# Optimization experiments

Measured on AMD Instinct MI355X. Metric: run time of the kernel, lower is better.

The kernel has to match this reference:

```python
import jax, jax.numpy as jnp
import numpy as np

CUTOFF = 0.5   # nm, matches init_kwargs cutoff
BOX = 5.0      # nm, orthogonal box edge length
N_ATOMS = 4096


def setup_inputs() -> dict:
    key = jax.random.key(0)
    positions = jax.random.uniform(key, (N_ATOMS, 3), dtype=jnp.float32) * BOX
    box_vectors = jnp.diag(jnp.full((3,), BOX, dtype=jnp.float32))  # [3,3] orthogonal box
    # upper-triangular unique pairs (i < j), same as torch meshgrid + mask
    i_np, j_np = np.triu_indices(N_ATOMS, k=1)
    i_pairs = jnp.asarray(i_np, dtype=jnp.int32)
    j_pairs = jnp.asarray(j_np, dtype=jnp.int32)
    return {"positions": positions, "box_vectors": box_vectors,
            "i_pairs": i_pairs, "j_pairs": j_pairs}


def reference(positions, box_vectors, i_pairs, j_pairs):
    """Brute-force N^2 neighborlist (unique pairs branch).

    Returns [n_pairs, 4]: columns 0:3 are r_ij displacement, column 3 is d_ij,
    with rows outside the cutoff zeroed (fixed-shape masking replaces the
    data-dependent boolean compaction of the torch original; the surviving
    values are identical).
    """
    # gather + displacement
    r_ij = positions[i_pairs] - positions[j_pairs]          # [P, 3]
    # periodic minimum-image wrap (orthogonal box: diagonal of box_vectors)
    box_lengths = jnp.diagonal(box_vectors)                 # [3]
    half = box_lengths * 0.5
    r_ij = jnp.remainder(r_ij + half, box_lengths) - half   # [P, 3]
    # distance
    d_ij = jnp.linalg.norm(r_ij, axis=1, keepdims=True)     # [P, 1]
    # cutoff mask (in-cutoff pairs kept, others zeroed)
    mask = (d_ij <= CUTOFF).astype(positions.dtype)         # [P, 1]
    return jnp.concatenate([r_ij, d_ij], axis=1) * mask     # [P, 4]
```

## Files before the change

kernel.cpp:

```cpp
#include <hip/hip_runtime.h>

#define N_ATOMS 4096
#define CUTOFF 0.5f

typedef float f32x4 __attribute__((ext_vector_type(4)));

__device__ __forceinline__ int row_start(int i) {
    return i * (N_ATOMS - 1) - (i * (i - 1)) / 2;
}

__global__ __launch_bounds__(256) void nbr_kernel(
    const float* __restrict__ pos,
    const float* __restrict__ box,
    f32x4* __restrict__ out,
    int n_pairs)
{
    const float Lx = box[0], Ly = box[4], Lz = box[8];
    const float hx = 0.5f * Lx, hy = 0.5f * Ly, hz = 0.5f * Lz;

    const int p = blockIdx.x * blockDim.x + threadIdx.x;
    if (p >= n_pairs) return;

    unsigned D = (2u * N_ATOMS - 1) * (2u * N_ATOMS - 1) - 8u * (unsigned)p;
    float t = sqrtf((float)D);
    int i = (int)(((float)(2 * N_ATOMS - 1) - t) * 0.5f);
    if (i < 0) i = 0;
    if (i > N_ATOMS - 2) i = N_ATOMS - 2;
    while (row_start(i + 1) <= p) ++i;
    while (row_start(i) > p) --i;
    const int j = p - row_start(i) + i + 1;

    const float xi = pos[3 * i], yi = pos[3 * i + 1], zi = pos[3 * i + 2];
    const float xj = pos[3 * j], yj = pos[3 * j + 1], zj = pos[3 * j + 2];

    float tx = (xi - xj) + hx;
    tx = (tx >= Lx) ? tx - Lx : tx;
    tx = (tx <  0.0f) ? tx + Lx : tx;
    float wx = tx - hx;

    float ty = (yi - yj) + hy;
    ty = (ty >= Ly) ? ty - Ly : ty;
    ty = (ty <  0.0f) ? ty + Ly : ty;
    float wy = ty - hy;

    float tz = (zi - zj) + hz;
    tz = (tz >= Lz) ? tz - Lz : tz;
    tz = (tz <  0.0f) ? tz + Lz : tz;
    float wz = tz - hz;

    const float d = sqrtf(wx * wx + wy * wy + wz * wz);
    const float m = (d <= CUTOFF) ? 1.0f : 0.0f;

    f32x4 v;
    v.x = wx * m; v.y = wy * m; v.z = wz * m; v.w = d * m;

    __builtin_nontemporal_store(v, &out[p]);
}

extern "C" void kernel_launch(void* const* d_in, const int* in_sizes, int n_in,
                              void* d_out, int out_size, void* d_ws, size_t ws_size,
                              hipStream_t stream) {
    const float* pos = (const float*)d_in[0];
    const float* box = (const float*)d_in[1];
    const int n_pairs = in_sizes[2];

    f32x4* out = (f32x4*)d_out;

    const int threads = 256;
    const int blocks = (n_pairs + threads - 1) / threads;

    nbr_kernel<<<blocks, threads, 0, stream>>>(pos, box, out, n_pairs);
}
```

Baseline: 171.3 us.

## Map one block per row i and loop over j instead of inverting pair index

Each block now handles one atom i and its threads stride over partner atoms j, so the sqrt-based row inversion and correction loops per pair go away. The i position is loaded once per block, and each j position is read with a vector load. The cost is heavy load imbalance across blocks, since row lengths shrink from 4095 down to 1, and the short rows leave most threads idle. Output writes stay contiguous within a row.

```diff
diff --git a/kernel.cpp b/kernel.cpp
--- a/kernel.cpp
+++ b/kernel.cpp
@@ -2,59 +2,56 @@
 
 #define N_ATOMS 4096
 #define CUTOFF 0.5f
+#define TPB 256
 
 typedef float f32x4 __attribute__((ext_vector_type(4)));
 
-__device__ __forceinline__ int row_start(int i) {
-    return i * (N_ATOMS - 1) - (i * (i - 1)) / 2;
-}
-
-__global__ __launch_bounds__(256) void nbr_kernel(
+__global__ __launch_bounds__(TPB) void nbr_kernel(
     const float* __restrict__ pos,
     const float* __restrict__ box,
-    f32x4* __restrict__ out,
-    int n_pairs)
+    f32x4* __restrict__ out)
 {
+    const int i = blockIdx.x;
+
     const float Lx = box[0], Ly = box[4], Lz = box[8];
     const float hx = 0.5f * Lx, hy = 0.5f * Ly, hz = 0.5f * Lz;
 
-    const int p = blockIdx.x * blockDim.x + threadIdx.x;
-    if (p >= n_pairs) return;
-
-    unsigned D = (2u * N_ATOMS - 1) * (2u * N_ATOMS - 1) - 8u * (unsigned)p;
-    float t = sqrtf((float)D);
-    int i = (int)(((float)(2 * N_ATOMS - 1) - t) * 0.5f);
-    if (i < 0) i = 0;
-    if (i > N_ATOMS - 2) i = N_ATOMS - 2;
-    while (row_start(i + 1) <= p) ++i;
-    while (row_start(i) > p) --i;
-    const int j = p - row_start(i) + i + 1;
+    const int r = i * (N_ATOMS - 1) - (i * (i - 1)) / 2;
 
     const float xi = pos[3 * i], yi = pos[3 * i + 1], zi = pos[3 * i + 2];
-    const float xj = pos[3 * j], yj = pos[3 * j + 1], zj = pos[3 * j + 2];
 
-    float tx = (xi - xj) + hx;
-    tx = (tx >= Lx) ? tx - Lx : tx;
-    tx = (tx <  0.0f) ? tx + Lx : tx;
-    float wx = tx - hx;
+    for (int j = i + 1 + (int)threadIdx.x; j < N_ATOMS; j += TPB) {
+        float xj, yj, zj;
+        if (j < N_ATOMS - 1) {
+            const f32x4 pj = *(const f32x4*)(pos + 3 * j);
+            xj = pj.x; yj = pj.y; zj = pj.z;
+        } else {
+            xj = pos[3 * j]; yj = pos[3 * j + 1]; zj = pos[3 * j + 2];
+        }
 
-    float ty = (yi - yj) + hy;
-    ty = (ty >= Ly) ? ty - Ly : ty;
-    ty = (ty <  0.0f) ? ty + Ly : ty;
-    float wy = ty - hy;
+        float tx = (xi - xj) + hx;
+        tx = (tx >= Lx) ? tx - Lx : tx;
+        tx = (tx <  0.0f) ? tx + Lx : tx;
+        const float wx = tx - hx;
 
-    float tz = (zi - zj) + hz;
-    tz = (tz >= Lz) ? tz - Lz : tz;
-    tz = (tz <  0.0f) ? tz + Lz : tz;
-    float wz = tz - hz;
+        float ty = (yi - yj) + hy;
+        ty = (ty >= Ly) ? ty - Ly : ty;
+        ty = (ty <  0.0f) ? ty + Ly : ty;
+        const float wy = ty - hy;
 
-    const float d = sqrtf(wx * wx + wy * wy + wz * wz);
-    const float m = (d <= CUTOFF) ? 1.0f : 0.0f;
+        float tz = (zi - zj) + hz;
+        tz = (tz >= Lz) ? tz - Lz : tz;
+        tz = (tz <  0.0f) ? tz + Lz : tz;
+        const float wz = tz - hz;
 
-    f32x4 v;
-    v.x = wx * m; v.y = wy * m; v.z = wz * m; v.w = d * m;
+        const float d = sqrtf(wx * wx + wy * wy + wz * wz);
+        const float m = (d <= CUTOFF) ? 1.0f : 0.0f;
 
-    __builtin_nontemporal_store(v, &out[p]);
+        f32x4 v;
+        v.x = wx * m; v.y = wy * m; v.z = wz * m; v.w = d * m;
+
+        __builtin_nontemporal_store(v, &out[r + (j - i - 1)]);
+    }
 }
 
 extern "C" void kernel_launch(void* const* d_in, const int* in_sizes, int n_in,
@@ -62,12 +59,8 @@
                               hipStream_t stream) {
     const float* pos = (const float*)d_in[0];
     const float* box = (const float*)d_in[1];
-    const int n_pairs = in_sizes[2];
 
     f32x4* out = (f32x4*)d_out;
 
-    const int threads = 256;
-    const int blocks = (n_pairs + threads - 1) / threads;
-
-    nbr_kernel<<<blocks, threads, 0, stream>>>(pos, box, out, n_pairs);
+    nbr_kernel<<<N_ATOMS - 1, TPB, 0, stream>>>(pos, box, out);
 }
```

Measured after the change: 182.1 us. +6.3%, slower.
